# Kernel optimization log

Measured on AMD Instinct MI355X. Metric: run time of the kernel, lower is better.

## Reference

```python
import jax, jax.numpy as jnp
from jax import lax
import numpy as np

V, E, NF = 50000, 300, 1          # vocab, embed_size, n_features
H = 256                            # hidden size (both layers)
B, TH, TB = 128, 32, 512           # batch, headline len, body len
NC = 4                             # n_classes


def setup_inputs() -> dict:
    key = jax.random.key(0)
    ks = jax.random.split(key, 24)
    emb = jax.random.normal(ks[0], (V, E), jnp.float32) * 0.1
    emb = emb.at[0].set(0.0)  # pad token -> zero row so seqlen masking is meaningful

    def make_ids(kid, klen, T):
        raw = jax.random.randint(kid, (B, T, NF), 1, V)
        lens = jax.random.randint(klen, (B,), max(T // 4, 1), T + 1)
        mask = jnp.arange(T)[None, :, None] < lens[:, None, None]
        return jnp.where(mask, raw, 0)

    headline_ids = make_ids(ks[1], ks[2], TH)
    body_ids = make_ids(ks[3], ks[4], TB)

    def gru_params(k, din, h):
        k1, k2 = jax.random.split(k, 2)
        s = 1.0 / np.sqrt(din + h)
        return (jax.random.normal(k1, (din + h, 2 * h), jnp.float32) * s,
                jnp.ones((2 * h,), jnp.float32),          # TF GRUCell gate bias init = 1.0
                jax.random.normal(k2, (din + h, h), jnp.float32) * s,
                jnp.zeros((h,), jnp.float32))

    D0 = NF * E
    hd0 = gru_params(ks[5], D0, H)
    hd1 = gru_params(ks[6], H, H)
    bd0 = gru_params(ks[7], D0, H)
    bd1 = gru_params(ks[8], H, H)

    W_pred = jax.random.normal(ks[9], (2 * H, NC), jnp.float32) * (1.0 / np.sqrt(2 * H))
    b_pred = jnp.zeros((NC,), jnp.float32)

    out = {"headline_ids": headline_ids, "body_ids": body_ids, "embeddings": emb,
           "W_pred": W_pred, "b_pred": b_pred}
    for pref, p in (("hd0", hd0), ("hd1", hd1), ("bd0", bd0), ("bd1", bd1)):
        out[pref + "_Wg"], out[pref + "_bg"], out[pref + "_Wc"], out[pref + "_bc"] = p
    return out


def _seq_length(x):
    # used = sign(max(|x|, axis=2)); seqlen = sum over time
    return jnp.sum(jnp.sign(jnp.max(jnp.abs(x), axis=2)), axis=1).astype(jnp.int32)


def _gru_layer(x, seqlen, Wg, bg, Wc, bc):
    # x: [B, T, D] -> outputs [B, T, H], final state [B, H]; dynamic_rnn semantics:
    # past seqlen, output is zero and state is copied through.
    Bsz, T, _ = x.shape
    Hh = Wc.shape[1]
    xt = jnp.swapaxes(x, 0, 1)  # [T, B, D]
    tids = jnp.arange(T)

    def step(h, inp):
        xi, t = inp
        xh = jnp.concatenate([xi, h], axis=-1)
        r, u = jnp.split(jax.nn.sigmoid(xh @ Wg + bg), 2, axis=-1)
        c = jnp.tanh(jnp.concatenate([xi, r * h], axis=-1) @ Wc + bc)
        nh = u * h + (1.0 - u) * c
        valid = (t < seqlen)[:, None]
        out = jnp.where(valid, nh, 0.0)
        h_next = jnp.where(valid, nh, h)
        return h_next, out

    h0 = jnp.zeros((Bsz, Hh), x.dtype)
    hf, outs = lax.scan(step, h0, (xt, tids))
    return jnp.swapaxes(outs, 0, 1), hf


def _stream(ids, emb, layers):
    x = emb[ids].reshape(ids.shape[0], ids.shape[1], -1)  # [B, T, NF*E]
    h = None
    for (Wg, bg, Wc, bc) in layers:
        sl = _seq_length(x)  # recomputed from current layer inputs, as in the source
        x, h = _gru_layer(x, sl, Wg, bg, Wc, bc)
    return h


def reference(headline_ids, body_ids, embeddings,
              hd0_Wg, hd0_bg, hd0_Wc, hd0_bc, hd1_Wg, hd1_bg, hd1_Wc, hd1_bc,
              bd0_Wg, bd0_bg, bd0_Wc, bd0_bc, bd1_Wg, bd1_bg, bd1_Wc, bd1_bc,
              W_pred, b_pred):
    h_head = _stream(headline_ids, embeddings,
                     [(hd0_Wg, hd0_bg, hd0_Wc, hd0_bc), (hd1_Wg, hd1_bg, hd1_Wc, hd1_bc)])
    h_body = _stream(body_ids, embeddings,
                     [(bd0_Wg, bd0_bg, bd0_Wc, bd0_bc), (bd1_Wg, bd1_bg, bd1_Wc, bd1_bc)])
    pred_input = jnp.concatenate([h_head, h_body], axis=1)  # [B, 2H]
    return pred_input @ W_pred + b_pred                      # [B, NC]
```

## Files before the change

kernel.cpp:

```cpp
#include <hip/hip_runtime.h>
#include <cstdint>
#include <cstddef>

#define H_    256
#define NG    768
#define BATCH 128
#define TH_   32
#define TB_   512
#define E_    300
#define RPB   16
#define CH_   16
#define NCH   32
#define NT_   192
#define NTRG  24
#define RING  4
#define NJ    72
#define NGRU  24
#define NWORK 168
#define NHEAT 32
#define GRID  (NGRU + NWORK + NHEAT)

#define G0S   ((size_t)BATCH * CH_ * NG)
#define OCS   ((size_t)BATCH * CH_ * H_)

#define F_QHEAD 0
#define F_CNT0  1
#define F_L0F   257
#define F_CNT1  513
#define F_L1F   769
#define F_HCNT0 1025
#define F_HL0F  1041
#define F_HCNT1 1057
#define F_DONE  1073
#define F_NUM   1074

typedef _Float16 half8 __attribute__((ext_vector_type(8)));
typedef _Float16 half4 __attribute__((ext_vector_type(4)));
typedef float    floatx4 __attribute__((ext_vector_type(4)));

#define AS1 __attribute__((address_space(1)))
#define AS3 __attribute__((address_space(3)))

#define WC_LGKM0 0xC07F
#define WCVM(N)  (0x0F70 | ((N) & 15) | (((N) >> 4) << 14))

__device__ __forceinline__ void hot_delay()
{
  float a = 1.f, b = 1.0000001f;
#pragma unroll
  for (int i = 0; i < 24; ++i) {
    asm volatile("v_fmac_f32 %0, %1, %1" : "+v"(a) : "v"(b));
    asm volatile("v_fmac_f32 %0, %1, %1" : "+v"(b) : "v"(a));
  }
}

__global__ __launch_bounds__(256) void pack_bias(
    const float* __restrict__ bg, const float* __restrict__ bc,
    float* __restrict__ bias)
{
  int idx = blockIdx.x * 256 + threadIdx.x;
  if (idx < NG) bias[idx] = (idx < 2 * H_) ? bg[idx] : bc[idx - 2 * H_];
}

__global__ __launch_bounds__(256) void pack_bx(
    const float* __restrict__ Wg, const float* __restrict__ Wc,
    int din, int KT, _Float16* __restrict__ out)
{
  int idx = blockIdx.x * 256 + threadIdx.x;
  if (idx >= KT * 48 * 64) return;
  int lane = idx & 63, tile = idx >> 6;
  int kt = tile / 48, nt = tile - kt * 48;
  int col = nt * 16 + (lane & 15);
  int k0 = kt * 32 + (lane >> 4) * 8;
  const float* W; int ncols, c2;
  if (col < 2 * H_) { W = Wg; ncols = 2 * H_; c2 = col; }
  else              { W = Wc; ncols = H_;     c2 = col - 2 * H_; }
  _Float16* dst = out + ((size_t)(kt * 48 + nt) * 64 + lane) * 8;
#pragma unroll
  for (int j = 0; j < 8; ++j) {
    int k = k0 + j;
    dst[j] = (k < din) ? (_Float16)W[(size_t)k * ncols + c2] : (_Float16)0.f;
  }
}

__global__ __launch_bounds__(256) void pack_w(
    const float* __restrict__ Wg, const float* __restrict__ Wc, int din,
    _Float16* __restrict__ wpk)
{
  int idx = blockIdx.x * 256 + threadIdx.x;
  if (idx >= 48 * 64) return;
  int tile = idx >> 6, lane = idx & 63;
  int grp = tile >> 4, tt = tile & 15;
  int wv = tt >> 1, s = tt & 1;
  const float* W; int ncols, n0;
  if (grp == 0)      { W = Wg; ncols = 2 * H_; n0 = wv * 32 + s * 16; }
  else if (grp == 1) { W = Wg; ncols = 2 * H_; n0 = 256 + wv * 32 + s * 16; }
  else               { W = Wc; ncols = H_;     n0 = wv * 32 + s * 16; }
  int n = n0 + (lane & 15);
  int kb = (lane >> 4) * 8;
#pragma unroll
  for (int kt = 0; kt < 8; ++kt) {
    _Float16* dst = wpk + ((size_t)(tile * 8 + kt) * 64 + lane) * 8;
#pragma unroll
    for (int j = 0; j < 8; ++j)
      dst[j] = (_Float16)W[(size_t)(din + kt * 32 + kb + j) * ncols + n];
  }
}

__global__ __launch_bounds__(256) void seq_k(const int* __restrict__ ids, int T,
                                             int* __restrict__ seq)
{
  __shared__ int red[256];
  int b = blockIdx.x, tid = threadIdx.x;
  int cnt = 0;
  for (int t = tid; t < T; t += 256) cnt += (ids[b * T + t] != 0) ? 1 : 0;
  red[tid] = cnt;
  __syncthreads();
  for (int s = 128; s > 0; s >>= 1) {
    if (tid < s) red[tid] += red[tid + s];
    __syncthreads();
  }
  if (tid == 0) seq[b] = red[0];
}

struct GemmJob {
  const _Float16* Adir; const int* ids; const _Float16* Bpk;
  const float* bias; _Float16* G;
  int K; int KT; int t0; int tcsh; int T;
};

struct PArgs {
  const float* emb; const int* idsH; const int* idsB;
  const int* seqH; const int* seqB;
  const _Float16 *Wpk0, *Wpk1, *Wpk2, *Wpk3;
  const _Float16 *Bx0, *Bx1, *Bx2, *Bx3;
  const float *bi0, *bi1, *bi2, *bi3;
  _Float16 *G0r, *G1r, *Ocr;
  _Float16 *GH0, *GH1, *OcH;
  float *hfH, *hfB;
  int* flg;
};

union SMem {
  struct { _Float16 hpk[4096]; _Float16 rpk[4096]; _Float16 Gs[4][12288]; } g;
  struct { _Float16 Al[2][64 * 40]; _Float16 Bl[2][8 * 512]; } m;
  struct { int bcast; int quit; } q;
};

__device__ __forceinline__ void gemm_block(const GemmJob& jb, const float* emb,
                                           int lb, SMem& sm)
{
  auto& Al = sm.m.Al;
  auto& Bl = sm.m.Bl;
  const int tid = threadIdx.x;
  const int w = tid >> 6, lane = tid & 63;
  const int quad = lane >> 4, l15 = lane & 15;
  const int gx = lb / 6, gy = lb - gx * 6;
  const int m0 = gx * 64, n0 = gy * 128;
  const int K = jb.K, KT = jb.KT, tcsh = jb.tcsh;
  const int tc = 1 << tcsh;

  const int am = tid >> 3, ak = tid & 7;
  const int arow = m0 + am;
  const _Float16* asrch = nullptr;
  const float*    asrcf = nullptr;
  if (jb.Adir) {
    asrch = jb.Adir + (size_t)arow * K;
  } else {
    int b = arow >> tcsh, tl = arow & (tc - 1);
    asrcf = emb + (size_t)jb.ids[b * jb.T + jb.t0 + tl] * K;
  }

  float a4[4];
  auto loadA = [&](int kt) {
    int k0 = kt * 32 + ak * 4;
    if (asrch) {
      half4 hv = *(const half4*)&asrch[k0];
#pragma unroll
      for (int j = 0; j < 4; ++j) a4[j] = (float)hv[j];
    } else {
#pragma unroll
      for (int j = 0; j < 4; ++j) a4[j] = (k0 + j < K) ? asrcf[k0 + j] : 0.f;
    }
  };
  auto writeA = [&](int buf) {
    half4 v;
#pragma unroll
    for (int j = 0; j < 4; ++j) v[j] = (_Float16)a4[j];
    *(half4*)&Al[buf][am * 40 + ak * 4] = v;
  };
  auto stageB = [&](int kt, int buf) {
    int nt = (n0 >> 4) + w;
    const _Float16* src = jb.Bpk + ((size_t)(kt * 48 + nt) * 64 + lane) * 8;
    __builtin_amdgcn_global_load_lds(
        (const AS1 unsigned int*)src,
        (AS3 unsigned int*)&Bl[buf][w * 512 + lane * 8], 16, 0, 0);
  };

  loadA(0);
  stageB(0, 0);
  writeA(0);
  floatx4 acc[4] = {};

  for (int kt = 0; kt < KT; ++kt) {
    const int buf = kt & 1;
    __syncthreads();
    if (kt + 1 < KT) { loadA(kt + 1); stageB(kt + 1, buf ^ 1); }
    half8 bf = *(const half8*)&Bl[buf][w * 512 + lane * 8];
#pragma unroll
    for (int st = 0; st < 4; ++st) {
      half8 af = *(const half8*)&Al[buf][(st * 16 + l15) * 40 + quad * 8];
      acc[st] = __builtin_amdgcn_mfma_f32_16x16x32_f16(af, bf, acc[st], 0, 0, 0);
    }
    if (kt + 1 < KT) writeA(buf ^ 1);
  }

  int col = n0 + w * 16 + l15;
  float bb = jb.bias[col];
  int g = col >> 8, kk = col & 255;
  int ww = kk >> 5, ss = (kk >> 4) & 1, ll = kk & 15;
  int cc = 2 * g + ss;
#pragma unroll
  for (int st = 0; st < 4; ++st) {
#pragma unroll
    for (int r = 0; r < 4; ++r) {
      int grow = m0 + st * 16 + quad * 4 + r;
      int b = grow >> tcsh, tl = grow & (tc - 1);
      int rg = b >> 4, mm = b & 15, qb = mm >> 2, rb = mm & 3;
      jb.G[((size_t)tl * BATCH + rg * RPB) * NG +
           ((ww * 6 + cc) * 64 + qb * 16 + ll) * 4 + rb] =
          (_Float16)(acc[st][r] + bb);
    }
  }
}

struct GruRun {
  const _Float16* W; const int* seq; int rg; int nch;
  const _Float16* Gb; size_t gs; int ring;
  _Float16* Ob; size_t os;
  float* stOut;
  int* wflag; int wtar;
  int* w2flag;
  int* pflag;
};

__device__ __forceinline__ void gru_run(const GruRun& P, SMem& sm)
{
  _Float16* hpk = sm.g.hpk;
  _Float16* rpk = sm.g.rpk;
  auto& Gs = sm.g.Gs;

  const int tid = threadIdx.x;
  const int w = tid >> 6, lane = tid & 63;
  const int quad = lane >> 4, l15 = lane & 15;

  floatx4 wg[4][8];
  floatx4 wc[2][8];
#pragma unroll
  for (int i = 0; i < 4; ++i) {
    const int tile = (i >> 1) * 16 + w * 2 + (i & 1);
#pragma unroll
    for (int kt = 0; kt < 8; ++kt) {
      wg[i][kt] = *(const floatx4*)&P.W[((size_t)(tile * 8 + kt) * 64 + lane) * 8];
      asm volatile("" : "+v"(wg[i][kt]));
    }
  }
#pragma unroll
  for (int i = 0; i < 2; ++i) {
    const int tile = 32 + w * 2 + i;
#pragma unroll
    for (int kt = 0; kt < 8; ++kt) {
      wc[i][kt] = *(const floatx4*)&P.W[((size_t)(tile * 8 + kt) * 64 + lane) * 8];
      asm volatile("" : "+a"(wc[i][kt]));
    }
  }

  int seq4[4];
#pragma unroll
  for (int r = 0; r < 4; ++r) seq4[r] = P.seq[P.rg * RPB + quad * 4 + r];
  int Smax = 0;
#pragma unroll
  for (int i = 0; i < 16; ++i) Smax = max(Smax, P.seq[P.rg * RPB + i]);

  const int wbase = (w * 64 + quad * 2 + (l15 >> 3)) * 8 + (l15 & 7);
  const int rbase = (((quad >> 1) << 5) + ((l15 & 3) << 3) +
                     ((l15 >> 2) << 1) + (quad & 1)) * 8;

  const bool dosnap = (P.stOut != nullptr);
  float h_reg[2][4], snap[2][4];
#pragma unroll
  for (int s = 0; s < 2; ++s)
#pragma unroll
    for (int r = 0; r < 4; ++r) {
      h_reg[s][r] = 0.f; snap[s][r] = 0.f;
      hpk[wbase + s * 256 + r * 64] = (_Float16)0.f;
    }

  const _Float16* hA = &hpk[rbase];
  const _Float16* rA = &rpk[rbase];

  for (int c = 0; c < P.nch; ++c) {
    if (tid == 0) {
      while (__hip_atomic_load(&P.wflag[c * 8 + P.rg], __ATOMIC_RELAXED,
                               __HIP_MEMORY_SCOPE_AGENT) < P.wtar)
        __builtin_amdgcn_s_sleep(2);
      if (P.w2flag && c >= RING)
        while (__hip_atomic_load(&P.w2flag[(c - RING) * 8 + P.rg],
                                 __ATOMIC_RELAXED,
                                 __HIP_MEMORY_SCOPE_AGENT) < NTRG)
          __builtin_amdgcn_s_sleep(2);
      __builtin_amdgcn_fence(__ATOMIC_ACQUIRE, "agent");
    }
    __syncthreads();

    const int slot = P.ring ? (c & (RING - 1)) : c;
    const _Float16* G = P.Gb + (size_t)slot * P.gs;
    _Float16* outp = P.Ob ? P.Ob + (size_t)slot * P.os : nullptr;
    const int t0 = c * CH_;
    int steps = Smax - t0;
    if (steps < 0) steps = 0;
    if (steps > CH_) steps = CH_;

    const _Float16* gblk = G + (size_t)P.rg * RPB * NG + w * 1536;
    _Float16* ldsw = &Gs[0][0] + w * 1536;
    auto stage = [&](int t, int buf) {
      const _Float16* gp = gblk + (size_t)t * BATCH * NG;
      _Float16* lp = ldsw + buf * 12288;
#pragma unroll
      for (int i = 0; i < 3; ++i) {
        __builtin_amdgcn_global_load_lds(
            (const AS1 unsigned int*)(gp + i * 512 + lane * 8),
            (AS3 unsigned int*)(lp + i * 512), 16, 0, 0);
      }
    };
    if (steps > 0) stage(0, 0);
    __syncthreads();
    if (steps > 1) stage(1, 1);
    if (steps > 2) stage(2, 2);

    for (int t = 0; t < steps; ++t) {
      const int buf = t & 3;

      {
        int np = outp ? ((t < 3) ? t : 3) : 0;
        int nf = steps - 1 - t; if (nf > 2) nf = 2;
        switch (np * 3 + nf) {
          case  0: __builtin_amdgcn_s_waitcnt(WCVM(0));  break;
          case  1: __builtin_amdgcn_s_waitcnt(WCVM(3));  break;
          case  2: __builtin_amdgcn_s_waitcnt(WCVM(6));  break;
          case  3: __builtin_amdgcn_s_waitcnt(WCVM(8));  break;
          case  4: __builtin_amdgcn_s_waitcnt(WCVM(11)); break;
          case  5: __builtin_amdgcn_s_waitcnt(WCVM(14)); break;
          case  6: __builtin_amdgcn_s_waitcnt(WCVM(16)); break;
          case  7: __builtin_amdgcn_s_waitcnt(WCVM(19)); break;
          case  8: __builtin_amdgcn_s_waitcnt(WCVM(22)); break;
          case  9: __builtin_amdgcn_s_waitcnt(WCVM(24)); break;
          case 10: __builtin_amdgcn_s_waitcnt(WCVM(27)); break;
          default: __builtin_amdgcn_s_waitcnt(WCVM(30)); break;
        }
      }

      half4 hga[6];
#pragma unroll
      for (int cc = 0; cc < 6; ++cc)
        hga[cc] = *(const half4*)&Gs[buf][(w * 6 + cc) * 256 + lane * 4];

      if (t + 3 < steps) stage(t + 3, (t + 3) & 3);

      floatx4 a0 = {}, a1 = {}, a0b = {}, a1b = {};
#pragma unroll
      for (int kt = 0; kt < 4; ++kt) {
        half8 a = *(const half8*)&hA[kt * 512];
        a0 = __builtin_amdgcn_mfma_f32_16x16x32_f16(
            a, __builtin_bit_cast(half8, wg[0][kt]), a0, 0, 0, 0);
        a1 = __builtin_amdgcn_mfma_f32_16x16x32_f16(
            a, __builtin_bit_cast(half8, wg[1][kt]), a1, 0, 0, 0);
      }
#pragma unroll
      for (int kt = 4; kt < 8; ++kt) {
        half8 a = *(const half8*)&hA[kt * 512];
        a0b = __builtin_amdgcn_mfma_f32_16x16x32_f16(
            a, __builtin_bit_cast(half8, wg[0][kt]), a0b, 0, 0, 0);
        a1b = __builtin_amdgcn_mfma_f32_16x16x32_f16(
            a, __builtin_bit_cast(half8, wg[1][kt]), a1b, 0, 0, 0);
      }
#pragma unroll
      for (int r = 0; r < 4; ++r) {
        float pre0 = a0[r] + a0b[r] + (float)hga[0][r];
        float g0 = __builtin_amdgcn_rcpf(1.f + __expf(-pre0));
        rpk[wbase + 0 * 256 + r * 64] = (_Float16)(g0 * h_reg[0][r]);
        float pre1 = a1[r] + a1b[r] + (float)hga[1][r];
        float g1 = __builtin_amdgcn_rcpf(1.f + __expf(-pre1));
        rpk[wbase + 1 * 256 + r * 64] = (_Float16)(g1 * h_reg[1][r]);
      }
      floatx4 a2 = {}, a3 = {};
#pragma unroll
      for (int kt = 0; kt < 8; ++kt) {
        half8 a = *(const half8*)&hA[kt * 512];
        a2 = __builtin_amdgcn_mfma_f32_16x16x32_f16(
            a, __builtin_bit_cast(half8, wg[2][kt]), a2, 0, 0, 0);
        a3 = __builtin_amdgcn_mfma_f32_16x16x32_f16(
            a, __builtin_bit_cast(half8, wg[3][kt]), a3, 0, 0, 0);
      }
      __builtin_amdgcn_s_waitcnt(WC_LGKM0);
      __builtin_amdgcn_s_barrier();

      floatx4 c0 = {}, c1 = {}, c2 = {}, c3 = {};
#pragma unroll
      for (int kt = 0; kt < 4; ++kt) {
        half8 a = *(const half8*)&rA[kt * 512];
        c0 = __builtin_amdgcn_mfma_f32_16x16x32_f16(
            a, __builtin_bit_cast(half8, wc[0][kt]), c0, 0, 0, 0);
        c2 = __builtin_amdgcn_mfma_f32_16x16x32_f16(
            a, __builtin_bit_cast(half8, wc[1][kt]), c2, 0, 0, 0);
      }
#pragma unroll
      for (int kt = 4; kt < 8; ++kt) {
        half8 a = *(const half8*)&rA[kt * 512];
        c1 = __builtin_amdgcn_mfma_f32_16x16x32_f16(
            a, __builtin_bit_cast(half8, wc[0][kt]), c1, 0, 0, 0);
        c3 = __builtin_amdgcn_mfma_f32_16x16x32_f16(
            a, __builtin_bit_cast(half8, wc[1][kt]), c3, 0, 0, 0);
      }
      float u_reg[2][4];
#pragma unroll
      for (int r = 0; r < 4; ++r) {
        u_reg[0][r] = __builtin_amdgcn_rcpf(
            1.f + __expf(-(a2[r] + (float)hga[2][r])));
        u_reg[1][r] = __builtin_amdgcn_rcpf(
            1.f + __expf(-(a3[r] + (float)hga[3][r])));
      }

#pragma unroll
      for (int s = 0; s < 2; ++s)
#pragma unroll
        for (int r = 0; r < 4; ++r) {
          float pre = (s == 0 ? c0[r] + c1[r] : c2[r] + c3[r]) +
                      (float)hga[4 + s][r];
          float cv = 1.f - 2.f * __builtin_amdgcn_rcpf(1.f + __expf(2.f * pre));
          float u = u_reg[s][r];
          float hn = u * h_reg[s][r] + (1.f - u) * cv;
          h_reg[s][r] = hn;
          hpk[wbase + s * 256 + r * 64] = (_Float16)hn;
        }
      if (dosnap) {
#pragma unroll
        for (int s = 0; s < 2; ++s)
#pragma unroll
          for (int r = 0; r < 4; ++r)
            snap[s][r] = (t0 + t + 1 == seq4[r]) ? h_reg[s][r] : snap[s][r];
      }
      if (outp) {
#pragma unroll
        for (int s = 0; s < 2; ++s)
#pragma unroll
          for (int r = 0; r < 4; ++r)
            outp[((size_t)(P.rg * RPB + quad * 4 + r) * CH_ + t) * H_ +
                 (w * 32 + s * 16 + l15)] = (_Float16)h_reg[s][r];
      }
      __builtin_amdgcn_s_waitcnt(WC_LGKM0);
      __builtin_amdgcn_s_barrier();
    }

    __syncthreads();
    if (P.pflag && tid == 0) {
      __builtin_amdgcn_fence(__ATOMIC_RELEASE, "agent");
      __hip_atomic_fetch_add(&P.pflag[c * 8 + P.rg], 1, __ATOMIC_RELAXED,
                             __HIP_MEMORY_SCOPE_AGENT);
    }
  }

  if (P.stOut) {
#pragma unroll
    for (int s = 0; s < 2; ++s)
#pragma unroll
      for (int r = 0; r < 4; ++r)
        P.stOut[(size_t)(P.rg * RPB + quad * 4 + r) * H_ +
                (w * 32 + s * 16 + l15)] = snap[s][r];
  }
}

__device__ __forceinline__ void worker(const PArgs& a, SMem& sm)
{
  int* flg = a.flg;
  for (;;) {
    if (threadIdx.x == 0)
      sm.q.bcast = __hip_atomic_fetch_add(&flg[F_QHEAD], 1, __ATOMIC_RELAXED,
                                          __HIP_MEMORY_SCOPE_AGENT);
    __syncthreads();
    int tile = sm.q.bcast;
    __syncthreads();
    if (tile >= NJ * NT_) return;
    int q = tile / NT_, lb = tile - q * NT_;
    int rg = (lb / 6) >> 2;

    GemmJob jb{};
    int* post = nullptr;
    int* d1 = nullptr;
    int* d2 = nullptr;
    bool skip = false;

    if (q < 4) {
      int c = q;
      jb = {nullptr, a.idsB, a.Bx2, a.bi2, a.G0r + (size_t)(c & 3) * G0S,
            E_, 10, c * CH_, 4, TB_};
      post = &flg[F_CNT0 + c * 8 + rg];
    } else if (q < 6) {
      int c = q - 4;
      jb = {nullptr, a.idsH, a.Bx0, a.bi0, a.GH0 + (size_t)c * G0S,
            E_, 10, c * CH_, 4, TH_};
      post = &flg[F_HCNT0 + c * 8 + rg];
    } else if (q < 8) {
      int c = q - 6;
      jb = {a.OcH + (size_t)c * OCS, nullptr, a.Bx1, a.bi1,
            a.GH1 + (size_t)c * G0S, H_, 8, 0, 4, TH_};
      d1 = &flg[F_HL0F + c * 8 + rg];
      post = &flg[F_HCNT1 + c * 8 + rg];
    } else {
      int k = (q - 8) >> 1;
      if (((q - 8) & 1) == 0) {
        jb = {a.Ocr + (size_t)(k & 3) * OCS, nullptr, a.Bx3, a.bi3,
              a.G1r + (size_t)(k & 3) * G0S, H_, 8, 0, 4, TB_};
        d1 = &flg[F_L0F + k * 8 + rg];
        if (k >= RING) d2 = &flg[F_L1F + (k - RING) * 8 + rg];
        post = &flg[F_CNT1 + k * 8 + rg];
      } else {
        int c = k + 4;
        if (c >= NCH) skip = true;
        else {
          jb = {nullptr, a.idsB, a.Bx2, a.bi2, a.G0r + (size_t)(c & 3) * G0S,
                E_, 10, c * CH_, 4, TB_};
          d1 = &flg[F_L0F + (c - RING) * 8 + rg];
          post = &flg[F_CNT0 + c * 8 + rg];
        }
      }
    }
    if (skip) continue;

    if (threadIdx.x == 0) {
      if (d1)
        while (__hip_atomic_load(d1, __ATOMIC_RELAXED,
                                 __HIP_MEMORY_SCOPE_AGENT) < 1)
          __builtin_amdgcn_s_sleep(8);
      if (d2)
        while (__hip_atomic_load(d2, __ATOMIC_RELAXED,
                                 __HIP_MEMORY_SCOPE_AGENT) < 1)
          __builtin_amdgcn_s_sleep(8);
      __builtin_amdgcn_fence(__ATOMIC_ACQUIRE, "agent");
    }
    __syncthreads();

    gemm_block(jb, a.emb, lb, sm);

    __syncthreads();
    if (threadIdx.x == 0) {
      __builtin_amdgcn_fence(__ATOMIC_RELEASE, "agent");
      __hip_atomic_fetch_add(post, 1, __ATOMIC_RELAXED,
                             __HIP_MEMORY_SCOPE_AGENT);
    }
  }
}

__device__ __forceinline__ void heater(const PArgs& a, SMem& sm)
{
  volatile int* qp = &sm.q.quit;
  if (threadIdx.x == 0) *qp = 0;
  __syncthreads();
  unsigned long long start = __builtin_amdgcn_s_memrealtime();
  for (;;) {
    hot_delay();
    if (threadIdx.x == 0) {
      bool done =
          __hip_atomic_load(&a.flg[F_DONE], __ATOMIC_RELAXED,
                            __HIP_MEMORY_SCOPE_AGENT) >= 8 ||
          (__builtin_amdgcn_s_memrealtime() - start) > 400000ull;
      if (done) *qp = 1;
    }
    if (*qp) break;
  }
}

__global__ __launch_bounds__(512, 1) void pers(PArgs a)
{
  __shared__ SMem sm;
  const int bid = blockIdx.x;
  int* flg = a.flg;

  if (bid < 8) {
    GruRun P{a.Wpk2, a.seqB, bid, NCH, a.G0r, G0S, 1,
             a.Ocr, OCS, nullptr,
             &flg[F_CNT0], NTRG, &flg[F_CNT1], &flg[F_L0F]};
    gru_run(P, sm);
  } else if (bid < 16) {
    GruRun P{a.Wpk3, a.seqB, bid - 8, NCH, a.G1r, G0S, 1,
             nullptr, 0, a.hfB,
             &flg[F_CNT1], NTRG, nullptr, &flg[F_L1F]};
    gru_run(P, sm);
    if (threadIdx.x == 0)
      __hip_atomic_fetch_add(&flg[F_DONE], 1, __ATOMIC_RELAXED,
                             __HIP_MEMORY_SCOPE_AGENT);
  } else if (bid < NGRU) {
    GruRun P0{a.Wpk0, a.seqH, bid - 16, 2, a.GH0, G0S, 0,
              a.OcH, OCS, nullptr,
              &flg[F_HCNT0], NTRG, nullptr, &flg[F_HL0F]};
    gru_run(P0, sm);
    GruRun P1{a.Wpk1, a.seqH, bid - 16, 2, a.GH1, G0S, 0,
              nullptr, 0, a.hfH,
              &flg[F_HCNT1], NTRG, nullptr, nullptr};
    gru_run(P1, sm);
  } else if (bid < NGRU + NWORK) {
    worker(a, sm);
  } else {
    heater(a, sm);
  }
}

__global__ __launch_bounds__(512) void pred_k(
    const float* __restrict__ hh, const float* __restrict__ hb,
    const float* __restrict__ Wp, const float* __restrict__ bpred,
    float* __restrict__ out)
{
  int tid = threadIdx.x;
  int b = tid >> 2, c = tid & 3;
  float acc = bpred[c];
  for (int k = 0; k < H_; ++k) acc += hh[b * H_ + k] * Wp[k * 4 + c];
  for (int k = 0; k < H_; ++k) acc += hb[b * H_ + k] * Wp[(H_ + k) * 4 + c];
  out[b * 4 + c] = acc;
}

extern "C" void kernel_launch(void* const* d_in, const int* in_sizes, int n_in,
                              void* d_out, int out_size, void* d_ws, size_t ws_size,
                              hipStream_t stream)
{
  (void)in_sizes; (void)n_in; (void)out_size; (void)ws_size;
  const int*   idsH = (const int*)  d_in[0];
  const int*   idsB = (const int*)  d_in[1];
  const float* emb  = (const float*)d_in[2];
  const float* Wp   = (const float*)d_in[3];
  const float* bp   = (const float*)d_in[4];
  const float* W[4][4];
  for (int s = 0; s < 4; ++s)
    for (int q = 0; q < 4; ++q)
      W[s][q] = (const float*)d_in[5 + s * 4 + q];

  float* wbase = (float*)d_ws;
  size_t off = 0;
  auto alloc = [&](size_t n) {
    float* p = wbase + off; off += (n + 255) & ~(size_t)255; return p;
  };

  int* flg = (int*)alloc(F_NUM);
  int* seqH = (int*)alloc(BATCH);
  int* seqB = (int*)alloc(BATCH);
  float* bi[4]; _Float16* Wpk[4]; _Float16* Bxh[4];
  const int din[4] = {E_, H_, E_, H_};
  const int KT[4]  = {10, 8, 10, 8};
  for (int s = 0; s < 4; ++s) {
    bi[s]  = alloc(NG);
    Wpk[s] = (_Float16*)alloc(48 * 8 * 64 * 8 / 2);
    Bxh[s] = (_Float16*)alloc((size_t)KT[s] * 48 * 64 * 8 / 2);
  }
  float* hfH = alloc((size_t)BATCH * H_);
  float* hfB = alloc((size_t)BATCH * H_);

  _Float16* GH0 = (_Float16*)alloc(2 * G0S / 2);
  _Float16* GH1 = (_Float16*)alloc(2 * G0S / 2);
  _Float16* OcH = (_Float16*)alloc(2 * OCS / 2);
  _Float16* G0r = (_Float16*)alloc(RING * G0S / 2);
  _Float16* G1r = (_Float16*)alloc(RING * G0S / 2);
  _Float16* Ocr = (_Float16*)alloc(RING * OCS / 2);

  hipMemsetAsync(flg, 0, F_NUM * sizeof(int), stream);

  for (int s = 0; s < 4; ++s) {
    pack_bias<<<(NG + 255) / 256, 256, 0, stream>>>(W[s][1], W[s][3], bi[s]);
    pack_w<<<(48 * 64 + 255) / 256, 256, 0, stream>>>(
        W[s][0], W[s][2], din[s], Wpk[s]);
    pack_bx<<<(KT[s] * 48 * 64 + 255) / 256, 256, 0, stream>>>(
        W[s][0], W[s][2], din[s], KT[s], Bxh[s]);
  }
  seq_k<<<BATCH, 256, 0, stream>>>(idsH, TH_, seqH);
  seq_k<<<BATCH, 256, 0, stream>>>(idsB, TB_, seqB);

  PArgs a;
  a.emb = emb; a.idsH = idsH; a.idsB = idsB; a.seqH = seqH; a.seqB = seqB;
  a.Wpk0 = Wpk[0]; a.Wpk1 = Wpk[1]; a.Wpk2 = Wpk[2]; a.Wpk3 = Wpk[3];
  a.Bx0 = Bxh[0]; a.Bx1 = Bxh[1]; a.Bx2 = Bxh[2]; a.Bx3 = Bxh[3];
  a.bi0 = bi[0]; a.bi1 = bi[1]; a.bi2 = bi[2]; a.bi3 = bi[3];
  a.G0r = G0r; a.G1r = G1r; a.Ocr = Ocr;
  a.GH0 = GH0; a.GH1 = GH1; a.OcH = OcH;
  a.hfH = hfH; a.hfB = hfB; a.flg = flg;
  pers<<<GRID, 512, 0, stream>>>(a);

  pred_k<<<1, 512, 0, stream>>>(hfH, hfB, Wp, bp, (float*)d_out);
}
```

Baseline: 2.082 ms.

## Fold weight packing and seqlen kernels into persistent kernel as flagged work items

Removes the 14 separate pack_bias/pack_w/pack_bx/seq_k launches and runs them as the first queue tiles in the persistent kernel's worker pool. GRU blocks and dependent GEMM tiles wait on new completion flags before consuming the packed weights and sequence lengths. The change also preloads the h/r fragments in a wave-rotated k order to spread LDS bank access, and switches sigmoid/tanh to exp2 with a log2e prescale. Launch overhead drops, but the first GEMM and GRU work now serialises behind in-kernel packing, and the fragment arrays raise register pressure.

```diff
diff --git a/kernel.cpp b/kernel.cpp
--- a/kernel.cpp
+++ b/kernel.cpp
@@ -15,6 +15,7 @@
 #define NTRG  24
 #define RING  4
 #define NJ    72
+#define NSET  34
 #define NGRU  24
 #define NWORK 168
 #define NHEAT 32
@@ -32,7 +33,9 @@
 #define F_HL0F  1041
 #define F_HCNT1 1057
 #define F_DONE  1073
-#define F_NUM   1074
+#define F_PK    1074
+#define F_SQ    1078
+#define F_NUM   1080
 
 typedef _Float16 half8 __attribute__((ext_vector_type(8)));
 typedef _Float16 half4 __attribute__((ext_vector_type(4)));
@@ -44,6 +47,13 @@
 #define WC_LGKM0 0xC07F
 #define WCVM(N)  (0x0F70 | ((N) & 15) | (((N) >> 4) << 14))
 
+#if __has_builtin(__builtin_amdgcn_exp2f)
+#define EXP2F(x) __builtin_amdgcn_exp2f(x)
+#else
+#define EXP2F(x) exp2f(x)
+#endif
+#define LOG2E 1.442695040f
+
 __device__ __forceinline__ void hot_delay()
 {
   float a = 1.f, b = 1.0000001f;
@@ -52,75 +62,6 @@
     asm volatile("v_fmac_f32 %0, %1, %1" : "+v"(a) : "v"(b));
     asm volatile("v_fmac_f32 %0, %1, %1" : "+v"(b) : "v"(a));
   }
-}
-
-__global__ __launch_bounds__(256) void pack_bias(
-    const float* __restrict__ bg, const float* __restrict__ bc,
-    float* __restrict__ bias)
-{
-  int idx = blockIdx.x * 256 + threadIdx.x;
-  if (idx < NG) bias[idx] = (idx < 2 * H_) ? bg[idx] : bc[idx - 2 * H_];
-}
-
-__global__ __launch_bounds__(256) void pack_bx(
-    const float* __restrict__ Wg, const float* __restrict__ Wc,
-    int din, int KT, _Float16* __restrict__ out)
-{
-  int idx = blockIdx.x * 256 + threadIdx.x;
-  if (idx >= KT * 48 * 64) return;
-  int lane = idx & 63, tile = idx >> 6;
-  int kt = tile / 48, nt = tile - kt * 48;
-  int col = nt * 16 + (lane & 15);
-  int k0 = kt * 32 + (lane >> 4) * 8;
-  const float* W; int ncols, c2;
-  if (col < 2 * H_) { W = Wg; ncols = 2 * H_; c2 = col; }
-  else              { W = Wc; ncols = H_;     c2 = col - 2 * H_; }
-  _Float16* dst = out + ((size_t)(kt * 48 + nt) * 64 + lane) * 8;
-#pragma unroll
-  for (int j = 0; j < 8; ++j) {
-    int k = k0 + j;
-    dst[j] = (k < din) ? (_Float16)W[(size_t)k * ncols + c2] : (_Float16)0.f;
-  }
-}
-
-__global__ __launch_bounds__(256) void pack_w(
-    const float* __restrict__ Wg, const float* __restrict__ Wc, int din,
-    _Float16* __restrict__ wpk)
-{
-  int idx = blockIdx.x * 256 + threadIdx.x;
-  if (idx >= 48 * 64) return;
-  int tile = idx >> 6, lane = idx & 63;
-  int grp = tile >> 4, tt = tile & 15;
-  int wv = tt >> 1, s = tt & 1;
-  const float* W; int ncols, n0;
-  if (grp == 0)      { W = Wg; ncols = 2 * H_; n0 = wv * 32 + s * 16; }
-  else if (grp == 1) { W = Wg; ncols = 2 * H_; n0 = 256 + wv * 32 + s * 16; }
-  else               { W = Wc; ncols = H_;     n0 = wv * 32 + s * 16; }
-  int n = n0 + (lane & 15);
-  int kb = (lane >> 4) * 8;
-#pragma unroll
-  for (int kt = 0; kt < 8; ++kt) {
-    _Float16* dst = wpk + ((size_t)(tile * 8 + kt) * 64 + lane) * 8;
-#pragma unroll
-    for (int j = 0; j < 8; ++j)
-      dst[j] = (_Float16)W[(size_t)(din + kt * 32 + kb + j) * ncols + n];
-  }
-}
-
-__global__ __launch_bounds__(256) void seq_k(const int* __restrict__ ids, int T,
-                                             int* __restrict__ seq)
-{
-  __shared__ int red[256];
-  int b = blockIdx.x, tid = threadIdx.x;
-  int cnt = 0;
-  for (int t = tid; t < T; t += 256) cnt += (ids[b * T + t] != 0) ? 1 : 0;
-  red[tid] = cnt;
-  __syncthreads();
-  for (int s = 128; s > 0; s >>= 1) {
-    if (tid < s) red[tid] += red[tid + s];
-    __syncthreads();
-  }
-  if (tid == 0) seq[b] = red[0];
 }
 
 struct GemmJob {
@@ -131,10 +72,12 @@
 
 struct PArgs {
   const float* emb; const int* idsH; const int* idsB;
-  const int* seqH; const int* seqB;
+  int* seqH; int* seqB;
   const _Float16 *Wpk0, *Wpk1, *Wpk2, *Wpk3;
   const _Float16 *Bx0, *Bx1, *Bx2, *Bx3;
   const float *bi0, *bi1, *bi2, *bi3;
+  const float* rW[4][4];
+  _Float16* wWpk[4]; _Float16* wBx[4]; float* wbi[4];
   _Float16 *G0r, *G1r, *Ocr;
   _Float16 *GH0, *GH1, *OcH;
   float *hfH, *hfB;
@@ -144,8 +87,75 @@
 union SMem {
   struct { _Float16 hpk[4096]; _Float16 rpk[4096]; _Float16 Gs[4][12288]; } g;
   struct { _Float16 Al[2][64 * 40]; _Float16 Bl[2][8 * 512]; } m;
-  struct { int bcast; int quit; } q;
+  struct { int bcast; int quit; int sred[512]; } q;
 };
+
+__device__ void pack_job(const PArgs& a, int s, int sub)
+{
+  const int tid = threadIdx.x;
+  const float* Wg = a.rW[s][0];
+  const float* bg = a.rW[s][1];
+  const float* Wc = a.rW[s][2];
+  const float* bc = a.rW[s][3];
+  const int din = (s & 1) ? H_ : E_;
+  const int KT  = (s & 1) ? 8 : 10;
+
+  if (sub == 0) {
+    for (int idx = tid; idx < NG; idx += 512)
+      a.wbi[s][idx] = (idx < 2 * H_) ? bg[idx] : bc[idx - 2 * H_];
+  }
+  if (tid < 384) {
+    int idx = sub * 384 + tid;
+    int tile = idx >> 6, lane = idx & 63;
+    int grp = tile >> 4, tt = tile & 15;
+    int wv = tt >> 1, ss = tt & 1;
+    const float* W; int ncols, n0;
+    if (grp == 0)      { W = Wg; ncols = 2 * H_; n0 = wv * 32 + ss * 16; }
+    else if (grp == 1) { W = Wg; ncols = 2 * H_; n0 = 256 + wv * 32 + ss * 16; }
+    else               { W = Wc; ncols = H_;     n0 = wv * 32 + ss * 16; }
+    int n = n0 + (lane & 15);
+    int kb = (lane >> 4) * 8;
+    _Float16* wpk = a.wWpk[s];
+#pragma unroll
+    for (int kt = 0; kt < 8; ++kt) {
+      _Float16* dst = wpk + ((size_t)(tile * 8 + kt) * 64 + lane) * 8;
+#pragma unroll
+      for (int j = 0; j < 8; ++j)
+        dst[j] = (_Float16)W[(size_t)(din + kt * 32 + kb + j) * ncols + n];
+    }
+  }
+  const int chunk = KT * 384;
+  for (int idx = sub * chunk + tid; idx < (sub + 1) * chunk; idx += 512) {
+    int lane = idx & 63, tile = idx >> 6;
+    int kt = tile / 48, nt = tile - kt * 48;
+    int col = nt * 16 + (lane & 15);
+    int k0 = kt * 32 + (lane >> 4) * 8;
+    const float* W; int ncols, c2;
+    if (col < 2 * H_) { W = Wg; ncols = 2 * H_; c2 = col; }
+    else              { W = Wc; ncols = H_;     c2 = col - 2 * H_; }
+    _Float16* dst = a.wBx[s] + ((size_t)(kt * 48 + nt) * 64 + lane) * 8;
+#pragma unroll
+    for (int j = 0; j < 8; ++j) {
+      int k = k0 + j;
+      dst[j] = (k < din) ? (_Float16)W[(size_t)k * ncols + c2] : (_Float16)0.f;
+    }
+  }
+}
+
+__device__ void seq_job(const int* __restrict__ ids, int T, int* __restrict__ seq,
+                        SMem& sm)
+{
+  int tid = threadIdx.x;
+  int row = tid >> 2, part = tid & 3;
+  int cnt = 0;
+  for (int t = part; t < T; t += 4) cnt += (ids[row * T + t] != 0) ? 1 : 0;
+  sm.q.sred[tid] = cnt;
+  __syncthreads();
+  if (part == 0)
+    seq[row] = sm.q.sred[tid] + sm.q.sred[tid + 1] +
+               sm.q.sred[tid + 2] + sm.q.sred[tid + 3];
+  __syncthreads();
+}
 
 __device__ __forceinline__ void gemm_block(const GemmJob& jb, const float* emb,
                                            int lb, SMem& sm)
@@ -367,68 +377,78 @@
 
       if (t + 3 < steps) stage(t + 3, (t + 3) & 3);
 
+      half8 hfrag[8];
+#pragma unroll
+      for (int kk = 0; kk < 8; ++kk)
+        hfrag[kk] = *(const half8*)&hA[(((kk + w) & 7)) * 512];
+
       floatx4 a0 = {}, a1 = {}, a0b = {}, a1b = {};
 #pragma unroll
-      for (int kt = 0; kt < 4; ++kt) {
-        half8 a = *(const half8*)&hA[kt * 512];
+      for (int kk = 0; kk < 4; ++kk) {
+        int kt = (kk + w) & 7;
         a0 = __builtin_amdgcn_mfma_f32_16x16x32_f16(
-            a, __builtin_bit_cast(half8, wg[0][kt]), a0, 0, 0, 0);
+            hfrag[kk], __builtin_bit_cast(half8, wg[0][kt]), a0, 0, 0, 0);
         a1 = __builtin_amdgcn_mfma_f32_16x16x32_f16(
-            a, __builtin_bit_cast(half8, wg[1][kt]), a1, 0, 0, 0);
-      }
-#pragma unroll
-      for (int kt = 4; kt < 8; ++kt) {
-        half8 a = *(const half8*)&hA[kt * 512];
+            hfrag[kk], __builtin_bit_cast(half8, wg[1][kt]), a1, 0, 0, 0);
+      }
+#pragma unroll
+      for (int kk = 4; kk < 8; ++kk) {
+        int kt = (kk + w) & 7;
         a0b = __builtin_amdgcn_mfma_f32_16x16x32_f16(
-            a, __builtin_bit_cast(half8, wg[0][kt]), a0b, 0, 0, 0);
+            hfrag[kk], __builtin_bit_cast(half8, wg[0][kt]), a0b, 0, 0, 0);
         a1b = __builtin_amdgcn_mfma_f32_16x16x32_f16(
-            a, __builtin_bit_cast(half8, wg[1][kt]), a1b, 0, 0, 0);
+            hfrag[kk], __builtin_bit_cast(half8, wg[1][kt]), a1b, 0, 0, 0);
       }
 #pragma unroll
       for (int r = 0; r < 4; ++r) {
         float pre0 = a0[r] + a0b[r] + (float)hga[0][r];
-        float g0 = __builtin_amdgcn_rcpf(1.f + __expf(-pre0));
-        rpk[wbase + 0 * 256 + r * 64] = (_Float16)(g0 * h_reg[0][r]);
+        float g0 = __builtin_amdgcn_rcpf(1.f + EXP2F(-LOG2E * pre0));
+        rpk[wbase + r * 64] = (_Float16)(g0 * h_reg[0][r]);
         float pre1 = a1[r] + a1b[r] + (float)hga[1][r];
-        float g1 = __builtin_amdgcn_rcpf(1.f + __expf(-pre1));
-        rpk[wbase + 1 * 256 + r * 64] = (_Float16)(g1 * h_reg[1][r]);
+        float g1 = __builtin_amdgcn_rcpf(1.f + EXP2F(-LOG2E * pre1));
+        rpk[wbase + 256 + r * 64] = (_Float16)(g1 * h_reg[1][r]);
       }
       floatx4 a2 = {}, a3 = {};
 #pragma unroll
-      for (int kt = 0; kt < 8; ++kt) {
-        half8 a = *(const half8*)&hA[kt * 512];
+      for (int kk = 0; kk < 8; ++kk) {
+        int kt = (kk + w) & 7;
         a2 = __builtin_amdgcn_mfma_f32_16x16x32_f16(
-            a, __builtin_bit_cast(half8, wg[2][kt]), a2, 0, 0, 0);
+            hfrag[kk], __builtin_bit_cast(half8, wg[2][kt]), a2, 0, 0, 0);
         a3 = __builtin_amdgcn_mfma_f32_16x16x32_f16(
-            a, __builtin_bit_cast(half8, wg[3][kt]), a3, 0, 0, 0);
+            hfrag[kk], __builtin_bit_cast(half8, wg[3][kt]), a3, 0, 0, 0);
       }
       __builtin_amdgcn_s_waitcnt(WC_LGKM0);
       __builtin_amdgcn_s_barrier();
 
+      half8 rfrag[8];
+#pragma unroll
+      for (int kk = 0; kk < 8; ++kk)
+        rfrag[kk] = *(const half8*)&rA[(((kk + w) & 7)) * 512];
+
       floatx4 c0 = {}, c1 = {}, c2 = {}, c3 = {};
 #pragma unroll
-      for (int kt = 0; kt < 4; ++kt) {
-        half8 a = *(const half8*)&rA[kt * 512];
+      for (int kk = 0; kk < 4; ++kk) {
+        int kt = (kk + w) & 7;
         c0 = __builtin_amdgcn_mfma_f32_16x16x32_f16(
-            a, __builtin_bit_cast(half8, wc[0][kt]), c0, 0, 0, 0);
+            rfrag[kk], __builtin_bit_cast(half8, wc[0][kt]), c0, 0, 0, 0);
         c2 = __builtin_amdgcn_mfma_f32_16x16x32_f16(
-            a, __builtin_bit_cast(half8, wc[1][kt]), c2, 0, 0, 0);
-      }
-#pragma unroll
-      for (int kt = 4; kt < 8; ++kt) {
-        half8 a = *(const half8*)&rA[kt * 512];
+            rfrag[kk], __builtin_bit_cast(half8, wc[1][kt]), c2, 0, 0, 0);
+      }
+#pragma unroll
+      for (int kk = 4; kk < 8; ++kk) {
+        int kt = (kk + w) & 7;
         c1 = __builtin_amdgcn_mfma_f32_16x16x32_f16(
-            a, __builtin_bit_cast(half8, wc[0][kt]), c1, 0, 0, 0);
+            rfrag[kk], __builtin_bit_cast(half8, wc[0][kt]), c1, 0, 0, 0);
         c3 = __builtin_amdgcn_mfma_f32_16x16x32_f16(
-            a, __builtin_bit_cast(half8, wc[1][kt]), c3, 0, 0, 0);
+            rfrag[kk], __builtin_bit_cast(half8, wc[1][kt]), c3, 0, 0, 0);
       }
       float u_reg[2][4];
 #pragma unroll
       for (int r = 0; r < 4; ++r) {
         u_reg[0][r] = __builtin_amdgcn_rcpf(
-            1.f + __expf(-(a2[r] + (float)hga[2][r])));
+            1.f + EXP2F(-LOG2E * (a2[r] + (float)hga[2][r])));
         u_reg[1][r] = __builtin_amdgcn_rcpf(
-            1.f + __expf(-(a3[r] + (float)hga[3][r])));
+            1.f + EXP2F(-LOG2E * (a3[r] + (float)hga[3][r])));
       }
 
 #pragma unroll
@@ -437,7 +457,8 @@
         for (int r = 0; r < 4; ++r) {
           float pre = (s == 0 ? c0[r] + c1[r] : c2[r] + c3[r]) +
                       (float)hga[4 + s][r];
-          float cv = 1.f - 2.f * __builtin_amdgcn_rcpf(1.f + __expf(2.f * pre));
+          float cv = 1.f - 2.f * __builtin_amdgcn_rcpf(
+                                     1.f + EXP2F(2.f * LOG2E * pre));
           float u = u_reg[s][r];
           float hn = u * h_reg[s][r] + (1.f - u) * cv;
           h_reg[s][r] = hn;
@@ -490,39 +511,66 @@
     __syncthreads();
     int tile = sm.q.bcast;
     __syncthreads();
-    if (tile >= NJ * NT_) return;
-    int q = tile / NT_, lb = tile - q * NT_;
+    if (tile >= NSET + NJ * NT_) return;
+
+    if (tile < NSET) {
+      int* post;
+      if (tile < 32) {
+        pack_job(a, tile >> 3, tile & 7);
+        post = &flg[F_PK + (tile >> 3)];
+      } else if (tile == 32) {
+        seq_job(a.idsH, TH_, a.seqH, sm);
+        post = &flg[F_SQ + 0];
+      } else {
+        seq_job(a.idsB, TB_, a.seqB, sm);
+        post = &flg[F_SQ + 1];
+      }
+      __syncthreads();
+      if (threadIdx.x == 0) {
+        __builtin_amdgcn_fence(__ATOMIC_RELEASE, "agent");
+        __hip_atomic_fetch_add(post, 1, __ATOMIC_RELAXED,
+                               __HIP_MEMORY_SCOPE_AGENT);
+      }
+      continue;
+    }
+
+    int t2 = tile - NSET;
+    int q = t2 / NT_, lb = t2 - q * NT_;
     int rg = (lb / 6) >> 2;
 
     GemmJob jb{};
     int* post = nullptr;
-    int* d1 = nullptr;
-    int* d2 = nullptr;
+    int* dp[3] = {nullptr, nullptr, nullptr};
+    int  dt[3] = {1, 1, 1};
     bool skip = false;
 
     if (q < 4) {
       int c = q;
       jb = {nullptr, a.idsB, a.Bx2, a.bi2, a.G0r + (size_t)(c & 3) * G0S,
             E_, 10, c * CH_, 4, TB_};
+      dp[0] = &flg[F_PK + 2]; dt[0] = 8;
       post = &flg[F_CNT0 + c * 8 + rg];
     } else if (q < 6) {
       int c = q - 4;
       jb = {nullptr, a.idsH, a.Bx0, a.bi0, a.GH0 + (size_t)c * G0S,
             E_, 10, c * CH_, 4, TH_};
+      dp[0] = &flg[F_PK + 0]; dt[0] = 8;
       post = &flg[F_HCNT0 + c * 8 + rg];
     } else if (q < 8) {
       int c = q - 6;
       jb = {a.OcH + (size_t)c * OCS, nullptr, a.Bx1, a.bi1,
             a.GH1 + (size_t)c * G0S, H_, 8, 0, 4, TH_};
-      d1 = &flg[F_HL0F + c * 8 + rg];
+      dp[0] = &flg[F_PK + 1]; dt[0] = 8;
+      dp[1] = &flg[F_HL0F + c * 8 + rg];
       post = &flg[F_HCNT1 + c * 8 + rg];
     } else {
       int k = (q - 8) >> 1;
       if (((q - 8) & 1) == 0) {
         jb = {a.Ocr + (size_t)(k & 3) * OCS, nullptr, a.Bx3, a.bi3,
               a.G1r + (size_t)(k & 3) * G0S, H_, 8, 0, 4, TB_};
-        d1 = &flg[F_L0F + k * 8 + rg];
-        if (k >= RING) d2 = &flg[F_L1F + (k - RING) * 8 + rg];
+        dp[0] = &flg[F_PK + 3]; dt[0] = 8;
+        dp[1] = &flg[F_L0F + k * 8 + rg];
+        if (k >= RING) dp[2] = &flg[F_L1F + (k - RING) * 8 + rg];
         post = &flg[F_CNT1 + k * 8 + rg];
       } else {
         int c = k + 4;
@@ -530,7 +578,7 @@
         else {
           jb = {nullptr, a.idsB, a.Bx2, a.bi2, a.G0r + (size_t)(c & 3) * G0S,
                 E_, 10, c * CH_, 4, TB_};
-          d1 = &flg[F_L0F + (c - RING) * 8 + rg];
+          dp[0] = &flg[F_L0F + (c - RING) * 8 + rg];
           post = &flg[F_CNT0 + c * 8 + rg];
         }
       }
@@ -538,14 +586,12 @@
     if (skip) continue;
 
     if (threadIdx.x == 0) {
-      if (d1)
-        while (__hip_atomic_load(d1, __ATOMIC_RELAXED,
-                                 __HIP_MEMORY_SCOPE_AGENT) < 1)
-          __builtin_amdgcn_s_sleep(8);
-      if (d2)
-        while (__hip_atomic_load(d2, __ATOMIC_RELAXED,
-                                 __HIP_MEMORY_SCOPE_AGENT) < 1)
-          __builtin_amdgcn_s_sleep(8);
+#pragma unroll
+      for (int k = 0; k < 3; ++k)
+        if (dp[k])
+          while (__hip_atomic_load(dp[k], __ATOMIC_RELAXED,
+                                   __HIP_MEMORY_SCOPE_AGENT) < dt[k])
+            __builtin_amdgcn_s_sleep(8);
       __builtin_amdgcn_fence(__ATOMIC_ACQUIRE, "agent");
     }
     __syncthreads();
@@ -586,12 +632,25 @@
   const int bid = blockIdx.x;
   int* flg = a.flg;
 
+  auto gwait = [&](int* f, int tgt) {
+    if (threadIdx.x == 0) {
+      while (__hip_atomic_load(f, __ATOMIC_RELAXED,
+                               __HIP_MEMORY_SCOPE_AGENT) < tgt)
+        __builtin_amdgcn_s_sleep(2);
+      __builtin_amdgcn_fence(__ATOMIC_ACQUIRE, "agent");
+    }
+  };
+
   if (bid < 8) {
+    gwait(&flg[F_PK + 2], 8); gwait(&flg[F_SQ + 1], 1);
+    __syncthreads();
     GruRun P{a.Wpk2, a.seqB, bid, NCH, a.G0r, G0S, 1,
              a.Ocr, OCS, nullptr,
              &flg[F_CNT0], NTRG, &flg[F_CNT1], &flg[F_L0F]};
     gru_run(P, sm);
   } else if (bid < 16) {
+    gwait(&flg[F_PK + 3], 8); gwait(&flg[F_SQ + 1], 1);
+    __syncthreads();
     GruRun P{a.Wpk3, a.seqB, bid - 8, NCH, a.G1r, G0S, 1,
              nullptr, 0, a.hfB,
              &flg[F_CNT1], NTRG, nullptr, &flg[F_L1F]};
@@ -600,6 +659,8 @@
       __hip_atomic_fetch_add(&flg[F_DONE], 1, __ATOMIC_RELAXED,
                              __HIP_MEMORY_SCOPE_AGENT);
   } else if (bid < NGRU) {
+    gwait(&flg[F_PK + 0], 8); gwait(&flg[F_PK + 1], 8); gwait(&flg[F_SQ + 0], 1);
+    __syncthreads();
     GruRun P0{a.Wpk0, a.seqH, bid - 16, 2, a.GH0, G0S, 0,
               a.OcH, OCS, nullptr,
               &flg[F_HCNT0], NTRG, nullptr, &flg[F_HL0F]};
@@ -638,10 +699,6 @@
   const float* emb  = (const float*)d_in[2];
   const float* Wp   = (const float*)d_in[3];
   const float* bp   = (const float*)d_in[4];
-  const float* W[4][4];
-  for (int s = 0; s < 4; ++s)
-    for (int q = 0; q < 4; ++q)
-      W[s][q] = (const float*)d_in[5 + s * 4 + q];
 
   float* wbase = (float*)d_ws;
   size_t off = 0;
@@ -653,7 +710,6 @@
   int* seqH = (int*)alloc(BATCH);
   int* seqB = (int*)alloc(BATCH);
   float* bi[4]; _Float16* Wpk[4]; _Float16* Bxh[4];
-  const int din[4] = {E_, H_, E_, H_};
   const int KT[4]  = {10, 8, 10, 8};
   for (int s = 0; s < 4; ++s) {
     bi[s]  = alloc(NG);
@@ -672,21 +728,15 @@
 
   hipMemsetAsync(flg, 0, F_NUM * sizeof(int), stream);
 
-  for (int s = 0; s < 4; ++s) {
-    pack_bias<<<(NG + 255) / 256, 256, 0, stream>>>(W[s][1], W[s][3], bi[s]);
-    pack_w<<<(48 * 64 + 255) / 256, 256, 0, stream>>>(
-        W[s][0], W[s][2], din[s], Wpk[s]);
-    pack_bx<<<(KT[s] * 48 * 64 + 255) / 256, 256, 0, stream>>>(
-        W[s][0], W[s][2], din[s], KT[s], Bxh[s]);
-  }
-  seq_k<<<BATCH, 256, 0, stream>>>(idsH, TH_, seqH);
-  seq_k<<<BATCH, 256, 0, stream>>>(idsB, TB_, seqB);
-
   PArgs a;
   a.emb = emb; a.idsH = idsH; a.idsB = idsB; a.seqH = seqH; a.seqB = seqB;
   a.Wpk0 = Wpk[0]; a.Wpk1 = Wpk[1]; a.Wpk2 = Wpk[2]; a.Wpk3 = Wpk[3];
   a.Bx0 = Bxh[0]; a.Bx1 = Bxh[1]; a.Bx2 = Bxh[2]; a.Bx3 = Bxh[3];
   a.bi0 = bi[0]; a.bi1 = bi[1]; a.bi2 = bi[2]; a.bi3 = bi[3];
+  for (int s = 0; s < 4; ++s) {
+    for (int q = 0; q < 4; ++q) a.rW[s][q] = (const float*)d_in[5 + s * 4 + q];
+    a.wWpk[s] = Wpk[s]; a.wBx[s] = Bxh[s]; a.wbi[s] = bi[s];
+  }
   a.G0r = G0r; a.G1r = G1r; a.Ocr = Ocr;
   a.GH0 = GH0; a.GH1 = GH1; a.OcH = OcH;
   a.hfH = hfH; a.hfB = hfB; a.flg = flg;
```

Result: slower. 5.323 ms (+155.7%).
